# Optimization experiments

Hardware: AMD Instinct MI355X
Metric: run time of the kernel (lower is better)

The kernel has to match this reference:

```python
import jax, jax.numpy as jnp
import numpy as np

HORIZON = 12
N_LAYERS = 2
HID = 256
DIM = 256
BATCH = 16384


def setup_inputs() -> dict:
    key = jax.random.key(0)
    ks = jax.random.split(key, 8)
    s = 0.05  # keep recurrence well-scaled
    return {
        "y0": jax.random.normal(ks[0], (BATCH, DIM), jnp.float32),
        "h0": jax.random.normal(ks[1], (N_LAYERS, BATCH, HID), jnp.float32),
        "W_ih": jax.random.normal(ks[2], (N_LAYERS, 3 * HID, DIM), jnp.float32) * s,
        "W_hh": jax.random.normal(ks[3], (N_LAYERS, 3 * HID, HID), jnp.float32) * s,
        "b_ih": jax.random.normal(ks[4], (N_LAYERS, 3 * HID), jnp.float32) * s,
        "b_hh": jax.random.normal(ks[5], (N_LAYERS, 3 * HID), jnp.float32) * s,
        "W_lin": jax.random.normal(ks[6], (DIM, HID), jnp.float32) * s,
        "b_lin": jax.random.normal(ks[7], (DIM,), jnp.float32) * s,
    }


def _gru_cell(x, h, Wih, Whh, bih, bhh):
    # torch.nn.GRUCell math
    gi = x @ Wih.T + bih  # [B, 3H]
    gh = h @ Whh.T + bhh  # [B, 3H]
    i_r, i_z, i_n = jnp.split(gi, 3, axis=-1)
    h_r, h_z, h_n = jnp.split(gh, 3, axis=-1)
    r = jax.nn.sigmoid(i_r + h_r)
    z = jax.nn.sigmoid(i_z + h_z)
    n = jnp.tanh(i_n + r * h_n)
    return (1.0 - z) * n + z * h


def reference(y0, h0, W_ih, W_hh, b_ih, b_hh, W_lin, b_lin):
    def step(carry, _):
        ytm1, ht = carry
        x = ytm1
        new_h = []
        for l in range(N_LAYERS):  # small fixed layer count
            hl = _gru_cell(x, ht[l], W_ih[l], W_hh[l], b_ih[l], b_hh[l])
            new_h.append(hl)
            x = hl
        ht = jnp.stack(new_h, axis=0)
        yt = x @ W_lin.T + b_lin  # linear(ht[-1])
        return (yt, ht), yt

    (_, _), yts = jax.lax.scan(step, (y0, h0), None, length=HORIZON)
    # torch.stack(yts, -3) with 2D yt -> [horizon, B, D]
    return yts
```

## Files before the change

### kernel.cpp

```cpp
#include <hip/hip_runtime.h>
#include <hip/hip_bf16.h>
#include <stdint.h>

#define HORIZON 12

typedef __bf16 bf16x8 __attribute__((ext_vector_type(8)));
typedef float  f32x16 __attribute__((ext_vector_type(16)));
typedef float  f32x4v __attribute__((ext_vector_type(4)));

__device__ __forceinline__ unsigned short f2bf(float f) {
  union { float f; uint32_t u; } v; v.f = f;
  return (unsigned short)((v.u + 0x7FFFu + ((v.u >> 16) & 1u)) >> 16);
}
__device__ __forceinline__ float bf2f(unsigned short s) {
  union { uint32_t u; float f; } v; v.u = ((uint32_t)s) << 16;
  return v.f;
}

__device__ __forceinline__ float sigm(float x) { return 1.0f / (1.0f + __expf(-x)); }
__device__ __forceinline__ float tanh_fast(float x) { return 1.0f - 2.0f / (__expf(2.0f * x) + 1.0f); }

#define MFMA(a, b, c) __builtin_amdgcn_mfma_f32_32x32x16_bf16(a, b, c, 0, 0, 0)

__global__ void prep(const float* __restrict__ wih, const float* __restrict__ whh,
                     const float* __restrict__ wlin, const float* __restrict__ bih,
                     const float* __restrict__ bhh, const float* __restrict__ blin,
                     unsigned short* __restrict__ Wb, float* __restrict__ Bc) {
  const int stride = gridDim.x * blockDim.x;
  for (int i = blockIdx.x * blockDim.x + threadIdx.x; i < 215296; i += stride) {
    if (i < 212992) {
      const int e = i << 2;
      const float* src; int m, rel;
      if (e < 196608)      { src = wih + e;             m = 0; rel = e; }
      else if (e < 393216) { src = whh + (e - 196608);  m = 1; rel = e - 196608; }
      else if (e < 589824) { src = wih + (e - 196608);  m = 2; rel = e - 393216; }
      else if (e < 786432) { src = whh + (e - 393216);  m = 3; rel = e - 589824; }
      else                 { src = wlin + (e - 786432); m = 4; rel = e - 786432; }
      const int rows = (m < 4) ? 768 : 256;
      const int r = rel >> 8, c = rel & 255;
      const float4 v = *(const float4*)src;
      unsigned short* dst = Wb + m * 196608 + ((c >> 4) * rows + r) * 16 + (c & 15);
      dst[0] = f2bf(v.x); dst[1] = f2bf(v.y); dst[2] = f2bf(v.z); dst[3] = f2bf(v.w);
    } else {
      const int t = i - 212992;
      float v;
      if (t < 512)       { const int l = t >> 8,        d = t & 255; v = bih[l*768+d]     + bhh[l*768+d]; }
      else if (t < 1024) { const int l = (t-512) >> 8,  d = t & 255; v = bih[l*768+256+d] + bhh[l*768+256+d]; }
      else if (t < 1536) { const int l = (t-1024) >> 8, d = t & 255; v = bih[l*768+512+d]; }
      else if (t < 2048) { const int l = (t-1536) >> 8, d = t & 255; v = bhh[l*768+512+d]; }
      else               { v = blin[t - 2048]; }
      Bc[t] = v;
    }
  }
}

__global__ __launch_bounds__(512) __attribute__((amdgpu_waves_per_eu(2, 2)))
void rnn_persist(
    const float* __restrict__ y0, const float* __restrict__ h0f,
    const unsigned short* __restrict__ Wb, const float* __restrict__ Bc,
    float* __restrict__ out) {
  extern __shared__ char lds[];
  char* XB = lds;
  char* H0 = lds + 32768;
  char* H1 = lds + 65536;
  char* SC = lds + 98304;

  const int tid = threadIdx.x;
  const int w   = tid >> 6;
  const int l   = tid & 63;
  const int l31 = l & 31;
  const int hi  = l >> 5;
  const int b0  = blockIdx.x * 64;
  const int dw  = w * 32 + l31;
  const int sub2 = (l31 & 7) * 2;
  const int gdw  = w * 4 + (l31 >> 3);

  f32x16 Ar[2], Az[2], Ai[2], Ah[2];

#pragma unroll
  for (int rr = 0; rr < 8; ++rr) {
    const int idx = rr * 2048 + tid * 4;
    const int row = idx >> 8, dd = idx & 255;
    const f32x4v v = __builtin_nontemporal_load(
        (const f32x4v*)(y0 + (size_t)(b0 + row) * 256 + dd));
    ushort4 o; o.x = f2bf(v.x); o.y = f2bf(v.y); o.z = f2bf(v.z); o.w = f2bf(v.w);
    *(ushort4*)(XB + row * 512 + (((dd >> 3) ^ (row & 31)) << 4) + (dd & 7) * 2) = o;
  }

  auto initH = [&](const float* src, char* Hl) {
#pragma unroll
    for (int rr = 0; rr < 8; ++rr) {
      const int idx = rr * 2048 + tid * 4;
      const int row = idx >> 8, dd = idx & 255;
      const f32x4v v = __builtin_nontemporal_load(
          (const f32x4v*)(src + (size_t)(b0 + row) * 256 + dd));
      ushort4 o; o.x = f2bf(v.x); o.y = f2bf(v.y); o.z = f2bf(v.z); o.w = f2bf(v.w);
      *(ushort4*)(Hl + row * 512 + (((dd >> 3) ^ (row & 31)) << 4) + (dd & 7) * 2) = o;
    }
  };
  initH(h0f, H0);
  initH(h0f + (size_t)16384 * 256, H1);
  __syncthreads();

  const char* Wp = (const char*)Wb;

  auto zacc = [&](f32x16 (&A)[2]) {
#pragma unroll
    for (int ct = 0; ct < 2; ++ct)
#pragma unroll
      for (int r = 0; r < 16; ++r) A[ct][r] = 0.0f;
  };

  auto passG3 = [&](const char* As, size_t mBase,
                    f32x16 (&G0)[2], f32x16 (&G1)[2], f32x16 (&G2)[2]) {
    const char* q0 = Wp + mBase + (size_t)(0 * 256 + dw) * 32 + hi * 16;
    const char* q1 = Wp + mBase + (size_t)(1 * 256 + dw) * 32 + hi * 16;
    const char* q2 = Wp + mBase + (size_t)(2 * 256 + dw) * 32 + hi * 16;
    bf16x8 f[5][3];
#define LOADSET3(buf)                                          \
    f[buf][0] = *(const bf16x8*)q0; q0 += 24576;               \
    f[buf][1] = *(const bf16x8*)q1; q1 += 24576;               \
    f[buf][2] = *(const bf16x8*)q2; q2 += 24576;               \
    asm volatile("" : "+v"(q0), "+v"(q1), "+v"(q2));
    LOADSET3(0)
    LOADSET3(1)
    LOADSET3(2)
    LOADSET3(3)
#pragma unroll
    for (int k = 0; k < 16; ++k) {
      if (k < 12) { LOADSET3((k + 4) % 5) }
      const int cur = k % 5;
      const int go = ((2 * k + hi) ^ l31) << 4;
      const bf16x8 a0 = *(const bf16x8*)(As + l31 * 512 + go);
      const bf16x8 a1 = *(const bf16x8*)(As + (32 + l31) * 512 + go);
      __builtin_amdgcn_s_setprio(1);
      G0[0] = MFMA(a0, f[cur][0], G0[0]);
      G1[0] = MFMA(a0, f[cur][1], G1[0]);
      G2[0] = MFMA(a0, f[cur][2], G2[0]);
      G0[1] = MFMA(a1, f[cur][0], G0[1]);
      G1[1] = MFMA(a1, f[cur][1], G1[1]);
      G2[1] = MFMA(a1, f[cur][2], G2[1]);
      __builtin_amdgcn_s_setprio(0);
    }
#undef LOADSET3
  };

  auto passLin = [&](const char* Hs, size_t mL) {
    const char* pL = Wp + mL + (size_t)dw * 32 + hi * 16;
    bf16x8 f[5];
#define LOADSET1(buf)                                          \
    f[buf] = *(const bf16x8*)pL; pL += 8192;                   \
    asm volatile("" : "+v"(pL));
    LOADSET1(0)
    LOADSET1(1)
    LOADSET1(2)
    LOADSET1(3)
#pragma unroll
    for (int k = 0; k < 16; ++k) {
      if (k < 12) { LOADSET1((k + 4) % 5) }
      const int cur = k % 5;
      const int go = ((2 * k + hi) ^ l31) << 4;
      const bf16x8 a0 = *(const bf16x8*)(Hs + l31 * 512 + go);
      const bf16x8 a1 = *(const bf16x8*)(Hs + (32 + l31) * 512 + go);
      __builtin_amdgcn_s_setprio(1);
      Ar[0] = MFMA(a0, f[cur], Ar[0]);
      Ar[1] = MFMA(a1, f[cur], Ar[1]);
      __builtin_amdgcn_s_setprio(0);
    }
#undef LOADSET1
  };

  auto epi = [&](int L, char* Hl) {
    const float brz = Bc[L * 256 + dw];
    const float bzz = Bc[512 + L * 256 + dw];
    const float bin = Bc[1024 + L * 256 + dw];
    const float bhn = Bc[1536 + L * 256 + dw];
#pragma unroll
    for (int ct = 0; ct < 2; ++ct) {
#pragma unroll
      for (int reg = 0; reg < 16; ++reg) {
        const int rl = (reg & 3) + 8 * (reg >> 2) + 4 * hi;
        unsigned short* hp =
            (unsigned short*)(Hl + (ct * 32 + rl) * 512 + ((gdw ^ rl) << 4) + sub2);
        const float hold = bf2f(*hp);
        const float rg = sigm(Ar[ct][reg] + brz);
        const float zg = sigm(Az[ct][reg] + bzz);
        const float nn = tanh_fast(Ai[ct][reg] + bin + rg * (Ah[ct][reg] + bhn));
        const float hv = (1.0f - zg) * nn + zg * hold;
        *hp = f2bf(hv);
      }
    }
  };

#pragma unroll 1
  for (int t = 0; t < HORIZON; ++t) {
    zacc(Ar); zacc(Az); zacc(Ai); zacc(Ah);
    passG3(XB, 0,      Ar, Az, Ai);
    passG3(H0, 393216, Ar, Az, Ah);
    __syncthreads();
    epi(0, H0);
    __syncthreads();
    zacc(Ar); zacc(Az); zacc(Ai); zacc(Ah);
    passG3(H0, 786432,  Ar, Az, Ai);
    passG3(H1, 1179648, Ar, Az, Ah);
    __syncthreads();
    epi(1, H1);
    __syncthreads();
    zacc(Ar);
    passLin(H1, 1572864);
    const float bl = Bc[2048 + dw];
#pragma unroll
    for (int ct = 0; ct < 2; ++ct) {
#pragma unroll
      for (int reg = 0; reg < 16; ++reg) {
        const int rl = (reg & 3) + 8 * (reg >> 2) + 4 * hi;
        *(float*)(SC + rl * 1024 + dw * 4) = Ar[ct][reg] + bl;
      }
      __syncthreads();
      float* og = out + ((size_t)t * 16384 + b0 + ct * 32) * 256;
#pragma unroll
      for (int rr = 0; rr < 4; ++rr) {
        const int idx = rr * 2048 + tid * 4;
        const int row = idx >> 8, dd = idx & 255;
        const f32x4v v = *(const f32x4v*)(SC + row * 1024 + dd * 4);
        __builtin_nontemporal_store(v, (f32x4v*)(og + row * 256 + dd));
        ushort4 o; o.x = f2bf(v.x); o.y = f2bf(v.y); o.z = f2bf(v.z); o.w = f2bf(v.w);
        const int xr = ct * 32 + row;
        *(ushort4*)(XB + xr * 512 + (((dd >> 3) ^ (xr & 31)) << 4) + (dd & 7) * 2) = o;
      }
      __syncthreads();
    }
  }
}

extern "C" void kernel_launch(void* const* d_in, const int* in_sizes, int n_in,
                              void* d_out, int out_size, void* d_ws, size_t ws_size,
                              hipStream_t stream) {
  (void)in_sizes; (void)n_in; (void)out_size; (void)ws_size;
  const float* y0   = (const float*)d_in[0];
  const float* h0   = (const float*)d_in[1];
  const float* wih  = (const float*)d_in[2];
  const float* whh  = (const float*)d_in[3];
  const float* bih  = (const float*)d_in[4];
  const float* bhh  = (const float*)d_in[5];
  const float* wlin = (const float*)d_in[6];
  const float* blin = (const float*)d_in[7];
  float* out = (float*)d_out;

  unsigned short* Wb = (unsigned short*)d_ws;
  float* Bc = (float*)((char*)d_ws + 1703936);

  static bool attr_done = false;
  if (!attr_done) {
    hipFuncSetAttribute((const void*)rnn_persist,
                        hipFuncAttributeMaxDynamicSharedMemorySize, 131072);
    attr_done = true;
  }

  prep<<<512, 256, 0, stream>>>(wih, whh, wlin, bih, bhh, blin, Wb, Bc);
  rnn_persist<<<256, 512, 131072, stream>>>(y0, h0, Wb, Bc, out);
}
```

Baseline: 630.5 us.

## Write outputs directly from MFMA registers, shrink weight prefetch, add per-step L2 warm

Drops the LDS staging buffer for the output linear layer: each lane now writes its MFMA accumulator values straight to global memory with scalar nontemporal stores and writes the bf16 feedback into XB directly. This removes two barriers per tile and cuts dynamic LDS from 128KB to 96KB. The weight register prefetch ring shrinks from depth 5 to 3 to lower register pressure. A per-step loop also has groups of 8 blocks each read a 52KB slice of the packed weights to warm cache, at the cost of extra loads and scalar uncoalesced-width stores.

```diff
diff --git a/kernel.cpp b/kernel.cpp
--- a/kernel.cpp
+++ b/kernel.cpp
@@ -63,7 +63,6 @@
   char* XB = lds;
   char* H0 = lds + 32768;
   char* H1 = lds + 65536;
-  char* SC = lds + 98304;
 
   const int tid = threadIdx.x;
   const int w   = tid >> 6;
@@ -116,7 +115,7 @@
     const char* q0 = Wp + mBase + (size_t)(0 * 256 + dw) * 32 + hi * 16;
     const char* q1 = Wp + mBase + (size_t)(1 * 256 + dw) * 32 + hi * 16;
     const char* q2 = Wp + mBase + (size_t)(2 * 256 + dw) * 32 + hi * 16;
-    bf16x8 f[5][3];
+    bf16x8 f[3][3];
 #define LOADSET3(buf)                                          \
     f[buf][0] = *(const bf16x8*)q0; q0 += 24576;               \
     f[buf][1] = *(const bf16x8*)q1; q1 += 24576;               \
@@ -124,12 +123,10 @@
     asm volatile("" : "+v"(q0), "+v"(q1), "+v"(q2));
     LOADSET3(0)
     LOADSET3(1)
-    LOADSET3(2)
-    LOADSET3(3)
 #pragma unroll
     for (int k = 0; k < 16; ++k) {
-      if (k < 12) { LOADSET3((k + 4) % 5) }
-      const int cur = k % 5;
+      if (k < 14) { LOADSET3((k + 2) % 3) }
+      const int cur = k % 3;
       const int go = ((2 * k + hi) ^ l31) << 4;
       const bf16x8 a0 = *(const bf16x8*)(As + l31 * 512 + go);
       const bf16x8 a1 = *(const bf16x8*)(As + (32 + l31) * 512 + go);
@@ -147,18 +144,18 @@
 
   auto passLin = [&](const char* Hs, size_t mL) {
     const char* pL = Wp + mL + (size_t)dw * 32 + hi * 16;
-    bf16x8 f[5];
-#define LOADSET1(buf)                                          \
-    f[buf] = *(const bf16x8*)pL; pL += 8192;                   \
+    bf16x8 f[3];
+    f[0] = *(const bf16x8*)pL; pL += 8192;
     asm volatile("" : "+v"(pL));
-    LOADSET1(0)
-    LOADSET1(1)
-    LOADSET1(2)
-    LOADSET1(3)
+    f[1] = *(const bf16x8*)pL; pL += 8192;
+    asm volatile("" : "+v"(pL));
 #pragma unroll
     for (int k = 0; k < 16; ++k) {
-      if (k < 12) { LOADSET1((k + 4) % 5) }
-      const int cur = k % 5;
+      if (k < 14) {
+        f[(k + 2) % 3] = *(const bf16x8*)pL; pL += 8192;
+        asm volatile("" : "+v"(pL));
+      }
+      const int cur = k % 3;
       const int go = ((2 * k + hi) ^ l31) << 4;
       const bf16x8 a0 = *(const bf16x8*)(Hs + l31 * 512 + go);
       const bf16x8 a1 = *(const bf16x8*)(Hs + (32 + l31) * 512 + go);
@@ -167,7 +164,6 @@
       Ar[1] = MFMA(a1, f[cur], Ar[1]);
       __builtin_amdgcn_s_setprio(0);
     }
-#undef LOADSET1
   };
 
   auto epi = [&](int L, char* Hl) {
@@ -194,6 +190,20 @@
 
 #pragma unroll 1
   for (int t = 0; t < HORIZON; ++t) {
+    {
+      const char* wbase = Wp + (size_t)(blockIdx.x >> 3) * 53248;
+      uint32_t acc = 0;
+#pragma unroll
+      for (int j = 0; j < 7; ++j) {
+        const int i = j * 512 + tid;
+        if (j < 6 || i < 3328) {
+          const uint4 wv = *(const uint4*)(wbase + (size_t)i * 16);
+          acc ^= wv.x ^ wv.y ^ wv.z ^ wv.w;
+        }
+      }
+      asm volatile("" :: "v"(acc));
+    }
+
     zacc(Ar); zacc(Az); zacc(Ai); zacc(Ah);
     passG3(XB, 0,      Ar, Az, Ai);
     passG3(H0, 393216, Ar, Az, Ah);
@@ -208,28 +218,22 @@
     __syncthreads();
     zacc(Ar);
     passLin(H1, 1572864);
-    const float bl = Bc[2048 + dw];
-#pragma unroll
-    for (int ct = 0; ct < 2; ++ct) {
-#pragma unroll
-      for (int reg = 0; reg < 16; ++reg) {
-        const int rl = (reg & 3) + 8 * (reg >> 2) + 4 * hi;
-        *(float*)(SC + rl * 1024 + dw * 4) = Ar[ct][reg] + bl;
-      }
-      __syncthreads();
-      float* og = out + ((size_t)t * 16384 + b0 + ct * 32) * 256;
-#pragma unroll
-      for (int rr = 0; rr < 4; ++rr) {
-        const int idx = rr * 2048 + tid * 4;
-        const int row = idx >> 8, dd = idx & 255;
-        const f32x4v v = *(const f32x4v*)(SC + row * 1024 + dd * 4);
-        __builtin_nontemporal_store(v, (f32x4v*)(og + row * 256 + dd));
-        ushort4 o; o.x = f2bf(v.x); o.y = f2bf(v.y); o.z = f2bf(v.z); o.w = f2bf(v.w);
-        const int xr = ct * 32 + row;
-        *(ushort4*)(XB + xr * 512 + (((dd >> 3) ^ (xr & 31)) << 4) + (dd & 7) * 2) = o;
-      }
-      __syncthreads();
-    }
+    {
+      const float bl = Bc[2048 + dw];
+      float* og = out + ((size_t)t * 16384 + b0) * 256;
+#pragma unroll
+      for (int ct = 0; ct < 2; ++ct) {
+#pragma unroll
+        for (int reg = 0; reg < 16; ++reg) {
+          const int rl = (reg & 3) + 8 * (reg >> 2) + 4 * hi;
+          const int row = ct * 32 + rl;
+          const float y = Ar[ct][reg] + bl;
+          __builtin_nontemporal_store(y, og + (size_t)row * 256 + dw);
+          *(unsigned short*)(XB + row * 512 + ((gdw ^ (row & 31)) << 4) + sub2) = f2bf(y);
+        }
+      }
+    }
+    __syncthreads();
   }
 }
 
@@ -253,10 +257,10 @@
   static bool attr_done = false;
   if (!attr_done) {
     hipFuncSetAttribute((const void*)rnn_persist,
-                        hipFuncAttributeMaxDynamicSharedMemorySize, 131072);
+                        hipFuncAttributeMaxDynamicSharedMemorySize, 98304);
     attr_done = true;
   }
 
   prep<<<512, 256, 0, stream>>>(wih, whh, wlin, bih, bhh, blin, Wb, Bc);
-  rnn_persist<<<256, 512, 131072, stream>>>(y0, h0, Wb, Bc, out);
-}
+  rnn_persist<<<256, 512, 98304, stream>>>(y0, h0, Wb, Bc, out);
+}
```

Result: slower. 653.7 us (+3.7%).
